# Performance work log

Hardware: AMD Instinct MI355X
Metric: run time of the kernel (lower is better)

## Reference

```python
import jax, jax.numpy as jnp
import numpy as np

B, S, D, H = 4, 2048, 1024, 16
DH = D // H  # 64


def setup_inputs() -> dict:
    key = jax.random.key(0)
    ks = jax.random.split(key, 9)
    scale = 1.0 / np.sqrt(D)
    x = jax.random.normal(ks[0], (B, S, D), dtype=jnp.float32)
    # Stacked per-head projection weights, equivalent to ModuleList of Linear(D, DH)
    Wq = jax.random.uniform(ks[1], (H, D, DH), jnp.float32, -scale, scale)
    bq = jax.random.uniform(ks[2], (H, DH), jnp.float32, -scale, scale)
    Wk = jax.random.uniform(ks[3], (H, D, DH), jnp.float32, -scale, scale)
    bk = jax.random.uniform(ks[4], (H, DH), jnp.float32, -scale, scale)
    Wv = jax.random.uniform(ks[5], (H, D, DH), jnp.float32, -scale, scale)
    bv = jax.random.uniform(ks[6], (H, DH), jnp.float32, -scale, scale)
    Wo = jax.random.uniform(ks[7], (D, D), jnp.float32, -scale, scale)
    bo = jax.random.uniform(ks[8], (D,), jnp.float32, -scale, scale)
    return {"x": x, "Wq": Wq, "bq": bq, "Wk": Wk, "bk": bk,
            "Wv": Wv, "bv": bv, "Wo": Wo, "bo": bo}


def reference(x, Wq, bq, Wk, bk, Wv, bv, Wo, bo):
    # Per-head Linear projections, batched across heads: [B,S,D]x[H,D,DH] -> [B,H,S,DH]
    q = jnp.einsum('bsd,hde->bhse', x, Wq) + bq[None, :, None, :]
    k = jnp.einsum('bsd,hde->bhse', x, Wk) + bk[None, :, None, :]
    v = jnp.einsum('bsd,hde->bhse', x, Wv) + bv[None, :, None, :]
    # Scaled dot-product attention (no mask is applied in the original forward)
    scores = jnp.einsum('bhse,bhte->bhst', q, k) / jnp.sqrt(jnp.float32(DH))
    attn = jax.nn.softmax(scores, axis=-1)
    z = jnp.einsum('bhst,bhte->bhse', attn, v)  # [B,H,S,DH]
    # Concat heads on last dim (head-major order matches torch.cat over dim=-1)
    multihead = jnp.transpose(z, (0, 2, 1, 3)).reshape(B, S, D)
    return multihead @ Wo + bo
```

## Files before the change

### kernel.cpp

```cpp
#include <hip/hip_runtime.h>
#include <hip/hip_bf16.h>
#include <cstdint>
#include <cstddef>


typedef unsigned short u16;
typedef unsigned int u32;
typedef __attribute__((ext_vector_type(8))) __bf16 bf16x8;
typedef __attribute__((ext_vector_type(8))) unsigned short u16x8;
typedef __attribute__((ext_vector_type(4))) float f32x4;
typedef __attribute__((ext_vector_type(4))) unsigned int u32x4;

__device__ __forceinline__ u16 f2bf(float f) {
  union { __hip_bfloat16 h; u16 u; } c;
  c.h = __float2bfloat16(f);
  return c.u;
}
#if defined(__has_builtin)
#if __has_builtin(__builtin_amdgcn_cvt_pk_bf16_f32)
#define HAS_PK_BF16 1
#endif
#endif
__device__ __forceinline__ u32 pk2c(float a, float b) {
#ifdef HAS_PK_BF16
  return __builtin_bit_cast(u32, __builtin_amdgcn_cvt_pk_bf16_f32(a, b));
#else
  const u32 ua = __float_as_uint(a);
  const u32 ub = __float_as_uint(b);
  const u32 ra = ua + 0x7FFFu + ((ua >> 16) & 1u);
  const u32 rb = ub + 0x7FFFu + ((ub >> 16) & 1u);
  return (ra >> 16) | (rb & 0xFFFF0000u);
#endif
}
__device__ __forceinline__ float ex2(float x) {
  return __builtin_amdgcn_exp2f(x);
}

__device__ __forceinline__ void async16(const void* g, void* l) {
  __builtin_amdgcn_global_load_lds(
      (const __attribute__((address_space(1))) void*)g,
      (__attribute__((address_space(3))) void*)l, 16, 0, 0);
}

__global__ void k_pack_all(const float* __restrict__ x,
                           const float* __restrict__ Wq, const float* __restrict__ Wk,
                           const float* __restrict__ Wv,
                           const float* __restrict__ bq, const float* __restrict__ bk,
                           const float* __restrict__ bv,
                           const float* __restrict__ Wo,
                           u16* __restrict__ xb, u16* __restrict__ Wt,
                           float* __restrict__ bqkv, u16* __restrict__ Wot) {
  __shared__ __align__(16) u16 tile[64][72];
  const int bid = blockIdx.x;
  const int t = threadIdx.x;
  if (bid < 1024) {
    const float* src;
    u16* dstp;
    int rstride, n_base, d0;
    if (bid < 768) {
      const int proj = bid >> 8, h = (bid >> 4) & 15, dt = bid & 15;
      const float* Wp = (proj == 0) ? Wq : ((proj == 1) ? Wk : Wv);
      src = Wp + h * 65536 + (dt * 64) * 64;
      rstride = 64;
      n_base = proj * 1024 + h * 64;
      d0 = dt * 64;
      dstp = Wt;
    } else {
      const int tb = bid - 768, nt = tb >> 4, dt = tb & 15;
      src = Wo + (size_t)(dt * 64) * 1024 + nt * 64;
      rstride = 1024;
      n_base = nt * 64;
      d0 = dt * 64;
      dstp = Wot;
    }
    {
      const int row = t >> 2, c0 = (t & 3) * 16;
      const float* s = src + row * rstride + c0;
#pragma unroll
      for (int j = 0; j < 4; ++j) {
        const float4 v = *(const float4*)(s + j * 4);
        ushort4 o;
        o.x = f2bf(v.x); o.y = f2bf(v.y); o.z = f2bf(v.z); o.w = f2bf(v.w);
        *(ushort4*)&tile[row][c0 + j * 4] = o;
      }
    }
    __syncthreads();
    {
      const int e = t >> 2, c0 = (t & 3) * 16;
      u16 buf[16];
#pragma unroll
      for (int i = 0; i < 16; ++i) buf[i] = tile[c0 + i][e];
      u16* d = dstp + (size_t)(n_base + e) * 1024 + d0 + c0;
      *(u16x8*)d = *(const u16x8*)&buf[0];
      *(u16x8*)(d + 8) = *(const u16x8*)&buf[8];
    }
  } else if (bid < 9216) {
    const int i = ((bid - 1024) * 256 + t) * 4;
    const float4 v = *(const float4*)(x + i);
    ushort4 o;
    o.x = f2bf(v.x); o.y = f2bf(v.y); o.z = f2bf(v.z); o.w = f2bf(v.w);
    *(ushort4*)(xb + i) = o;
  } else {
    const int n = (bid - 9216) * 256 + t;
    const int proj = n >> 10, rem = n & 1023, h = rem >> 6, e = rem & 63;
    const float* bp = (proj == 0) ? bq : ((proj == 1) ? bk : bv);
    bqkv[n] = bp[h * 64 + e];
  }
}

template <int MODE>
__global__ __launch_bounds__(256)
void k_gemm(const u16* __restrict__ A, const u16* __restrict__ Bt,
            const float* __restrict__ bias, void* __restrict__ Cout, int ldc) {
  __shared__ __align__(16) u16 Alds[2][4096];
  __shared__ __align__(16) u16 Blds[2][4096];
  const int t = threadIdx.x;
  const int lane = t & 63;
  const int w = t >> 6;
  const int l15 = lane & 15;
  const int quad = lane >> 4;
  const int wm = w >> 1, wn = w & 1;

  const int nwg = gridDim.x * gridDim.y;
  const int wg  = blockIdx.y * gridDim.x + blockIdx.x;
  const int q8  = nwg >> 3;
  const int swz = (wg & 7) * q8 + (wg >> 3);
  const int bx  = swz % gridDim.x;
  const int by  = swz / gridDim.x;
  const int m0 = by << 7;
  const int n0 = bx << 7;

  const u16* ga0 = A + (size_t)(m0 + (t >> 2)) * 1024 + (t & 3) * 8;
  const u16* ga1 = ga0 + (size_t)64 * 1024;
  const u16* gb0 = Bt + (size_t)(n0 + (t >> 2)) * 1024 + (t & 3) * 8;
  const u16* gb1 = gb0 + (size_t)64 * 1024;
  const int lofs0 = w * 512;
  const int lofs1 = w * 512 + 2048;

  f32x4 acc[4][4];
#pragma unroll
  for (int mi = 0; mi < 4; ++mi)
#pragma unroll
    for (int ni = 0; ni < 4; ++ni) acc[mi][ni] = (f32x4){0.f, 0.f, 0.f, 0.f};

  async16(ga0, &Alds[0][lofs0]); async16(ga1, &Alds[0][lofs1]);
  async16(gb0, &Blds[0][lofs0]); async16(gb1, &Blds[0][lofs1]);
  ga0 += 32; ga1 += 32; gb0 += 32; gb1 += 32;

#define GEMM_COMPUTE(BUF)                                                     \
  {                                                                           \
    const u16* const Ab = &Alds[BUF][0];                                      \
    const u16* const Bb = &Blds[BUF][0];                                      \
    bf16x8 af[4], bfr[4];                                                     \
    _Pragma("unroll")                                                         \
    for (int i = 0; i < 4; ++i) {                                             \
      af[i]  = *(const bf16x8*)(Ab + (wm * 64 + i * 16 + l15) * 32 + quad * 8); \
      bfr[i] = *(const bf16x8*)(Bb + (wn * 64 + i * 16 + l15) * 32 + quad * 8); \
    }                                                                         \
    _Pragma("unroll")                                                         \
    for (int mi = 0; mi < 4; ++mi)                                            \
      _Pragma("unroll")                                                       \
      for (int ni = 0; ni < 4; ++ni)                                          \
        acc[mi][ni] = __builtin_amdgcn_mfma_f32_16x16x32_bf16(                \
            af[mi], bfr[ni], acc[mi][ni], 0, 0, 0);                           \
  }

#pragma unroll 2
  for (int kt = 0; kt < 31; ++kt) {
    const int cur = kt & 1, nxt = cur ^ 1;
    __builtin_amdgcn_s_barrier();
    async16(ga0, &Alds[nxt][lofs0]); async16(ga1, &Alds[nxt][lofs1]);
    async16(gb0, &Blds[nxt][lofs0]); async16(gb1, &Blds[nxt][lofs1]);
    ga0 += 32; ga1 += 32; gb0 += 32; gb1 += 32;
    asm volatile("s_waitcnt vmcnt(4)" ::: "memory");
    __builtin_amdgcn_s_barrier();
    __builtin_amdgcn_sched_barrier(0);
    GEMM_COMPUTE(cur);
  }
  asm volatile("s_waitcnt vmcnt(0)" ::: "memory");
  __builtin_amdgcn_s_barrier();
  __builtin_amdgcn_sched_barrier(0);
  GEMM_COMPUTE(1);
#undef GEMM_COMPUTE

  const int row0 = m0 + wm * 64;
  const int col0 = n0 + wn * 64;
  const float qscale = (MODE == 0 && col0 < 1024) ? 0.125f * 1.4426950408889634f : 1.0f;
#pragma unroll
  for (int mi = 0; mi < 4; ++mi) {
#pragma unroll
    for (int ni = 0; ni < 4; ++ni) {
      const int col = col0 + ni * 16 + l15;
      const float bb = bias[col];
#pragma unroll
      for (int r = 0; r < 4; ++r) {
        const int row = row0 + mi * 16 + quad * 4 + r;
        const float v = (acc[mi][ni][r] + bb) * qscale;
        if (MODE == 0) ((u16*)Cout)[(size_t)row * ldc + col] = f2bf(v);
        else           ((float*)Cout)[(size_t)row * ldc + col] = v;
      }
    }
  }
}

__global__ __launch_bounds__(256)
void k_vt(const u16* __restrict__ qkv, u16* __restrict__ vtg) {
  __shared__ u16 tile[64][72];
  const int t = threadIdx.x;
  const int bh = blockIdx.y, b = bh >> 4, h = bh & 15;
  const int s0 = blockIdx.x << 6;
  {
    const int row = t >> 2, col0 = (t & 3) * 16;
    const u16* src = qkv + (size_t)(b * 2048 + s0 + row) * 3072 + 2048 + h * 64 + col0;
    const u16x8 v0 = *(const u16x8*)src;
    const u16x8 v1 = *(const u16x8*)(src + 8);
    *(u16x8*)&tile[row][col0] = v0;
    *(u16x8*)&tile[row][col0 + 8] = v1;
  }
  __syncthreads();
  {
    const int e = t >> 2, sc = (t & 3) * 16;
    u16 buf[16];
#pragma unroll
    for (int i = 0; i < 16; ++i) buf[i] = tile[sc + i][e];
    u16* dst = vtg + ((size_t)bh * 64 + e) * 2048 + s0 + sc;
    *(u16x8*)dst = *(const u16x8*)&buf[0];
    *(u16x8*)(dst + 8) = *(const u16x8*)&buf[8];
  }
}

__global__ __launch_bounds__(256)
void k_attn(const u16* __restrict__ qkv, const u16* __restrict__ vtg,
            u16* __restrict__ mh) {
  __shared__ __align__(16) u16 smem[16384];

  const int t = threadIdx.x;
  const int lane = t & 63;
  const int w = t >> 6;
  const int l15 = lane & 15;
  const int quad = lane >> 4;
  const int bh = blockIdx.x, b = bh >> 4, h = bh & 15;
  const int s0 = blockIdx.y << 7;

  const int lam0 = t >> 3;
  const int key0 = (lam0 & 3) | (((lam0 >> 2) & 3) << 3) | (((lam0 >> 4) & 1) << 2);
  const int ck = (t & 7) ^ (lam0 & 7);
  const u16* kbase = qkv + (size_t)(b * 2048 + key0) * 3072 + 1024 + h * 64 + ck * 8;
  const int e0 = t >> 3;
  const int cv = (t & 7) ^ (e0 & 7);
  const u16* vbase = vtg + ((size_t)bh * 64 + e0) * 2048 + cv * 8;

  const int kofs = w * 512;
  const int vofs = 4096 + w * 512;

  bf16x8 aq[2][2];
#pragma unroll
  for (int g = 0; g < 2; ++g)
#pragma unroll
    for (int ks2 = 0; ks2 < 2; ++ks2)
      aq[g][ks2] = *(const bf16x8*)(qkv +
          (size_t)(b * 2048 + s0 + w * 32 + g * 16 + l15) * 3072 +
          h * 64 + ks2 * 32 + quad * 8);

  const u32x4 onesu = (u32x4){0x3F803F80u, 0x3F803F80u, 0x3F803F80u, 0x3F803F80u};
  const bf16x8 ones = __builtin_bit_cast(bf16x8, onesu);

  f32x4 o[2][4];
  f32x4 lacc[2];
#pragma unroll
  for (int g = 0; g < 2; ++g) {
    lacc[g] = (f32x4){0.f, 0.f, 0.f, 0.f};
#pragma unroll
    for (int ne = 0; ne < 4; ++ne) o[g][ne] = (f32x4){0.f, 0.f, 0.f, 0.f};
  }

#pragma unroll
  for (int r = 0; r < 2; ++r) {
    async16(kbase + (size_t)r * (32 * 3072), smem + kofs + r * 2048);
    async16(vbase + (size_t)r * (32 * 2048), smem + vofs + r * 2048);
  }
  kbase += 64 * 3072;
  vbase += 64;

#pragma unroll 2
  for (int kt = 0; kt < 32; ++kt) {
    const int cur = kt & 1;
    const u16* const Kc = smem + cur * 8192;
    const u16* const Vc = Kc + 4096;
    u16* const nb = smem + (cur ^ 1) * 8192;

    __builtin_amdgcn_s_barrier();
#pragma unroll
    for (int r = 0; r < 2; ++r) {
      async16(kbase + (size_t)r * (32 * 3072), nb + kofs + r * 2048);
      async16(vbase + (size_t)r * (32 * 2048), nb + vofs + r * 2048);
    }
    kbase += 64 * 3072;
    vbase += 64;
    asm volatile("s_waitcnt vmcnt(4)" ::: "memory");
    __builtin_amdgcn_s_barrier();
    __builtin_amdgcn_sched_barrier(0);

#pragma unroll
    for (int ks = 0; ks < 2; ++ks) {
      u32x4 pf[2];
#pragma unroll
      for (int h2 = 0; h2 < 2; ++h2) {
        const int row = (ks * 2 + h2) * 16 + l15;
        const bf16x8 kf0 = *(const bf16x8*)(Kc + row * 64 + ((quad) ^ (l15 & 7)) * 8);
        const bf16x8 kf1 = *(const bf16x8*)(Kc + row * 64 + ((4 + quad) ^ (l15 & 7)) * 8);
        f32x4 st[2];
        __builtin_amdgcn_s_setprio(1);
#pragma unroll
        for (int g = 0; g < 2; ++g) {
          st[g] = __builtin_amdgcn_mfma_f32_16x16x32_bf16(kf0, aq[g][0], (f32x4){0.f,0.f,0.f,0.f}, 0, 0, 0);
          st[g] = __builtin_amdgcn_mfma_f32_16x16x32_bf16(kf1, aq[g][1], st[g], 0, 0, 0);
        }
        __builtin_amdgcn_s_setprio(0);
#pragma unroll
        for (int g = 0; g < 2; ++g) {
          const float p0 = ex2(st[g][0]), p1 = ex2(st[g][1]);
          const float p2 = ex2(st[g][2]), p3 = ex2(st[g][3]);
          pf[g][h2 * 2 + 0] = pk2c(p0, p1);
          pf[g][h2 * 2 + 1] = pk2c(p2, p3);
        }
      }
      __builtin_amdgcn_s_setprio(1);
#pragma unroll
      for (int ne = 0; ne < 4; ++ne) {
        const int e = ne * 16 + l15;
        const bf16x8 bv8 = *(const bf16x8*)(Vc + e * 64 + ((ks * 4 + quad) ^ (e & 7)) * 8);
#pragma unroll
        for (int g = 0; g < 2; ++g)
          o[g][ne] = __builtin_amdgcn_mfma_f32_16x16x32_bf16(
              __builtin_bit_cast(bf16x8, pf[g]), bv8, o[g][ne], 0, 0, 0);
      }
#pragma unroll
      for (int g = 0; g < 2; ++g)
        lacc[g] = __builtin_amdgcn_mfma_f32_16x16x32_bf16(
            __builtin_bit_cast(bf16x8, pf[g]), ones, lacc[g], 0, 0, 0);
      __builtin_amdgcn_s_setprio(0);
    }
  }

#pragma unroll
  for (int g = 0; g < 2; ++g) {
#pragma unroll
    for (int r = 0; r < 4; ++r) {
      const float iv = 1.f / lacc[g][r];
      const int row = s0 + w * 32 + g * 16 + quad * 4 + r;
#pragma unroll
      for (int ne = 0; ne < 4; ++ne) {
        const int col = h * 64 + ne * 16 + l15;
        mh[(size_t)(b * 2048 + row) * 1024 + col] = f2bf(o[g][ne][r] * iv);
      }
    }
  }
}

extern "C" void kernel_launch(void* const* d_in, const int* in_sizes, int n_in,
                              void* d_out, int out_size, void* d_ws, size_t ws_size,
                              hipStream_t stream) {
  (void)in_sizes; (void)n_in; (void)out_size; (void)ws_size;
  const float* x  = (const float*)d_in[0];
  const float* Wq = (const float*)d_in[1];
  const float* bq = (const float*)d_in[2];
  const float* Wk = (const float*)d_in[3];
  const float* bk = (const float*)d_in[4];
  const float* Wv = (const float*)d_in[5];
  const float* bv = (const float*)d_in[6];
  const float* Wo = (const float*)d_in[7];
  const float* bo = (const float*)d_in[8];

  char* ws = (char*)d_ws;
  u16*   Xb   = (u16*)  (ws + 0);
  u16*   Vtg  = (u16*)  (ws + 0);
  u16*   Wt   = (u16*)  (ws + 16777216);
  float* bqkv = (float*)(ws + 23068672);
  u16*   Wot  = (u16*)  (ws + 23080960);
  u16*   QKV  = (u16*)  (ws + 25178112);
  u16*   MH   = (u16*)  (ws + 75509760);
  float* out  = (float*)d_out;

  k_pack_all <<<9228, 256, 0, stream>>>(x, Wq, Wk, Wv, bq, bk, bv, Wo,
                                        Xb, Wt, bqkv, Wot);
  k_gemm<0>  <<<dim3(24, 64), 256, 0, stream>>>(Xb, Wt, bqkv, (void*)QKV, 3072);
  k_vt       <<<dim3(32, 64), 256, 0, stream>>>(QKV, Vtg);
  k_attn     <<<dim3(64, 16), 256, 0, stream>>>(QKV, Vtg, MH);
  k_gemm<1>  <<<dim3(8, 64), 256, 0, stream>>>(MH, Wot, bo, (void*)out, 1024);
}
```

Measured before the change: 282.2 us.

## Add 256x256-tile 512-thread GEMM kernel for fused QKV projection

Replaces the QKV projection GEMM with a new kernel that uses 256x256 output tiles, 8 waves per workgroup, and a double-buffered async LDS pipeline with 32-wide K steps. Larger tiles increase operand reuse per global load and cut global/L2 traffic relative to the 128x128 version. The trade-offs are higher register pressure (128 accumulator floats per thread), 64KB of LDS per block, and a grid of only 384 blocks, which may underfill the GPU's compute units.

Result: no change. 286.6 us (+1.6%).

```diff
diff --git a/kernel.cpp b/kernel.cpp
--- a/kernel.cpp
+++ b/kernel.cpp
@@ -108,6 +108,113 @@
   }
 }
 
+__global__ __launch_bounds__(512)
+void k_gemm256(const u16* __restrict__ A, const u16* __restrict__ Bt,
+               const float* __restrict__ bias, u16* __restrict__ Cout, int ldc) {
+  __shared__ __align__(16) u16 Alds[2][8192];
+  __shared__ __align__(16) u16 Blds[2][8192];
+  const int t = threadIdx.x;
+  const int lane = t & 63;
+  const int w = t >> 6;
+  const int l15 = lane & 15;
+  const int quad = lane >> 4;
+  const int wm = w >> 2, wn = w & 3;
+
+  const int nwg = gridDim.x * gridDim.y;
+  const int wg  = blockIdx.y * gridDim.x + blockIdx.x;
+  const int q8  = nwg >> 3;
+  const int swz = (wg & 7) * q8 + (wg >> 3);
+  const int bx  = swz % gridDim.x;
+  const int by  = swz / gridDim.x;
+  const int m0 = by << 8;
+  const int n0 = bx << 8;
+
+  const int p3   = lane >> 3;
+  const int s    = (lane & 7) ^ p3;
+  const int rloc = w * 16 + 2 * p3 + (s >> 2);
+  const int cloc = (s & 3) * 8;
+  const u16* gA = A  + (size_t)(m0 + rloc) * 1024 + cloc;
+  const u16* gB = Bt + (size_t)(n0 + rloc) * 1024 + cloc;
+  const int ldst = w * 512;
+
+  const int pr = l15 >> 1;
+  const int sl = (((l15 & 1) << 2) + quad) ^ (pr & 7);
+  const int abase = (wm * 64 + pr) * 64 + sl * 8;
+  const int bbase = (wn * 32 + pr) * 64 + sl * 8;
+
+  f32x4 acc[8][4];
+#pragma unroll
+  for (int mi = 0; mi < 8; ++mi)
+#pragma unroll
+    for (int ni = 0; ni < 4; ++ni) acc[mi][ni] = (f32x4){0.f, 0.f, 0.f, 0.f};
+
+#define STAGE256(BUF)                                          \
+  async16(gA,              &Alds[BUF][ldst]);                  \
+  async16(gA + 128 * 1024, &Alds[BUF][4096 + ldst]);           \
+  async16(gB,              &Blds[BUF][ldst]);                  \
+  async16(gB + 128 * 1024, &Blds[BUF][4096 + ldst]);           \
+  gA += 32; gB += 32;
+
+#define COMPUTE256(BUF)                                                       \
+  {                                                                           \
+    bf16x8 bf[4];                                                             \
+    _Pragma("unroll")                                                         \
+    for (int ni = 0; ni < 4; ++ni)                                            \
+      bf[ni] = *(const bf16x8*)(&Blds[BUF][bbase + ni * 512]);                \
+    _Pragma("unroll")                                                         \
+    for (int mh = 0; mh < 2; ++mh) {                                          \
+      bf16x8 af[4];                                                           \
+      _Pragma("unroll")                                                       \
+      for (int q = 0; q < 4; ++q)                                             \
+        af[q] = *(const bf16x8*)(&Alds[BUF][abase + (mh * 4 + q) * 512]);     \
+      __builtin_amdgcn_s_setprio(1);                                          \
+      _Pragma("unroll")                                                       \
+      for (int q = 0; q < 4; ++q)                                             \
+        _Pragma("unroll")                                                     \
+        for (int ni = 0; ni < 4; ++ni)                                        \
+          acc[mh * 4 + q][ni] = __builtin_amdgcn_mfma_f32_16x16x32_bf16(      \
+              af[q], bf[ni], acc[mh * 4 + q][ni], 0, 0, 0);                   \
+      __builtin_amdgcn_s_setprio(0);                                         \
+    }                                                                         \
+  }
+
+  STAGE256(0)
+
+#pragma unroll 2
+  for (int kt = 0; kt < 31; ++kt) {
+    const int cur = kt & 1, nxt = cur ^ 1;
+    __builtin_amdgcn_s_barrier();
+    STAGE256(nxt)
+    asm volatile("s_waitcnt vmcnt(4)" ::: "memory");
+    __builtin_amdgcn_s_barrier();
+    __builtin_amdgcn_sched_barrier(0);
+    COMPUTE256(cur)
+  }
+  asm volatile("s_waitcnt vmcnt(0)" ::: "memory");
+  __builtin_amdgcn_s_barrier();
+  __builtin_amdgcn_sched_barrier(0);
+  COMPUTE256(1)
+#undef STAGE256
+#undef COMPUTE256
+
+  const int row0 = m0 + wm * 128;
+  const int col0 = n0 + wn * 64;
+  const float qscale = (col0 < 1024) ? 0.125f * 1.4426950408889634f : 1.0f;
+#pragma unroll
+  for (int mi = 0; mi < 8; ++mi) {
+#pragma unroll
+    for (int ni = 0; ni < 4; ++ni) {
+      const int col = col0 + ni * 16 + l15;
+      const float bb = bias[col];
+#pragma unroll
+      for (int r = 0; r < 4; ++r) {
+        const int row = row0 + mi * 16 + quad * 4 + r;
+        Cout[(size_t)row * ldc + col] = f2bf((acc[mi][ni][r] + bb) * qscale);
+      }
+    }
+  }
+}
+
 template <int MODE>
 __global__ __launch_bounds__(256)
 void k_gemm(const u16* __restrict__ A, const u16* __restrict__ Bt,
@@ -384,7 +491,7 @@
 
   k_pack_all <<<9228, 256, 0, stream>>>(x, Wq, Wk, Wv, bq, bk, bv, Wo,
                                         Xb, Wt, bqkv, Wot);
-  k_gemm<0>  <<<dim3(24, 64), 256, 0, stream>>>(Xb, Wt, bqkv, (void*)QKV, 3072);
+  k_gemm256  <<<dim3(12, 32), 512, 0, stream>>>(Xb, Wt, bqkv, QKV, 3072);
   k_vt       <<<dim3(32, 64), 256, 0, stream>>>(QKV, Vtg);
   k_attn     <<<dim3(64, 16), 256, 0, stream>>>(QKV, Vtg, MH);
   k_gemm<1>  <<<dim3(8, 64), 256, 0, stream>>>(MH, Wot, bo, (void*)out, 1024);
```
